# Optimization experiments

Hardware: AMD Instinct MI355X
Metric: run time of the kernel (lower is better)

Reference implementation:

```python
import math
import jax, jax.numpy as jnp
import numpy as np

INPUT_DIM = 512
HIDDEN_DIM = 512
BATCH = 8
SEQ_LEN = 4096


def _xavier(key, shape):
    fan_out, fan_in = shape
    limit = math.sqrt(6.0 / (fan_in + fan_out))
    return jax.random.uniform(key, shape, jnp.float32, -limit, limit)


def setup_inputs() -> dict:
    key = jax.random.key(0)
    kx, kA, kB, kC, kD, kWg = jax.random.split(key, 6)
    return {
        "x": jax.random.normal(kx, (BATCH, SEQ_LEN, INPUT_DIM), jnp.float32),
        "A": jax.random.uniform(kA, (HIDDEN_DIM,), jnp.float32, 0.8, 0.95),
        "B": _xavier(kB, (HIDDEN_DIM, INPUT_DIM)),
        "C": _xavier(kC, (HIDDEN_DIM, HIDDEN_DIM)),
        "D": _xavier(kD, (HIDDEN_DIM, INPUT_DIM)),
        "Wg": _xavier(kWg, (HIDDEN_DIM, INPUT_DIM)),
        "bias_h": jnp.zeros((HIDDEN_DIM,), jnp.float32),
        "bias_y": jnp.zeros((HIDDEN_DIM,), jnp.float32),
    }


def reference(x, A, B, C, D, Wg, bias_h, bias_y):
    # x: (b, t, i). Eval mode: dropout is identity.
    hidden_dim = A.shape[0]
    # Precompute all input-dependent per-step terms as batched GEMMs.
    g = jnp.clip(jax.nn.sigmoid(jnp.einsum('bti,hi->bth', x, Wg)), 0.05, 0.95)
    xB = jnp.einsum('bti,hi->bth', x, B)
    # h_t = h_{t-1} + g_t*(A*h_{t-1} + xB_t + bias_h - h_{t-1})
    #     = (1 - g_t*(1 - A)) * h_{t-1} + g_t*(xB_t + bias_h)
    a_coef = 1.0 - g * (1.0 - A)          # (b, t, h)
    b_coef = g * (xB + bias_h)            # (b, t, h)

    def step(h, ab):
        a_t, b_t = ab
        h = a_t * h + b_t
        return h, h

    h0 = jnp.zeros((x.shape[0], hidden_dim), x.dtype)
    _, hs = jax.lax.scan(step, h0, (jnp.swapaxes(a_coef, 0, 1), jnp.swapaxes(b_coef, 0, 1)))
    hs = jnp.swapaxes(hs, 0, 1)           # (b, t, h)

    scale = 1.0 / math.sqrt(hidden_dim)
    y = (jnp.einsum('bth,oh->bto', hs, C) + jnp.einsum('bti,hi->bth', x, D) + bias_y) * scale
    return y
```

## Files before the change

kernel.cpp:

```cpp
#include <hip/hip_runtime.h>
#include <math.h>

#define MTOT 32768
#define KD 512
#define HD 512
#define NB 8
#define TS 4096
#define NCHUNK 64
#define TCHUNK 64

typedef __attribute__((ext_vector_type(8))) short bf16x8;
typedef __attribute__((ext_vector_type(4))) float f32x4;
typedef __attribute__((ext_vector_type(4))) unsigned short us4;

#define GLD16(gsrc, ldst) __builtin_amdgcn_global_load_lds( \
    (const __attribute__((address_space(1))) void*)(gsrc),   \
    (__attribute__((address_space(3))) void*)(ldst), 16, 0, 0)

__device__ __forceinline__ unsigned short f2bf(float f) {
    unsigned u = __float_as_uint(f);
    return (unsigned short)((u + 0x7FFFu + ((u >> 16) & 1u)) >> 16);
}
__device__ __forceinline__ float bf2f(unsigned short u) {
    return __uint_as_float(((unsigned)u) << 16);
}

__global__ __launch_bounds__(256) void cast_x(const float* __restrict__ src,
                                              unsigned short* __restrict__ dst) {
    const int i = (blockIdx.x * 256 + threadIdx.x) * 4;
    float4 v = *(const float4*)(src + i);
    us4 o; o.x = f2bf(v.x); o.y = f2bf(v.y); o.z = f2bf(v.z); o.w = f2bf(v.w);
    *(us4*)(dst + i) = o;
}

__global__ __launch_bounds__(256) void cast_w(const float* __restrict__ B,
                                              const float* __restrict__ D,
                                              const float* __restrict__ G,
                                              const float* __restrict__ C,
                                              unsigned short* __restrict__ dst) {
    const float* srcs[4] = {B, D, G, C};
    const float* s = srcs[blockIdx.y];
    unsigned short* d = dst + (size_t)blockIdx.y * (HD * KD);
    const int i = (blockIdx.x * 256 + threadIdx.x) * 4;
    float4 v = *(const float4*)(s + i);
    us4 o; o.x = f2bf(v.x); o.y = f2bf(v.y); o.z = f2bf(v.z); o.w = f2bf(v.w);
    *(us4*)(d + i) = o;
}

__global__ __launch_bounds__(256, 2) void in_gemm_mfma(
    const short* __restrict__ xb, const short* __restrict__ wmat,
    const float* __restrict__ Avec, const float* __restrict__ bias_h,
    unsigned* __restrict__ ab16, unsigned short* __restrict__ xd16,
    float2* __restrict__ chPS)
{
    __shared__ __align__(16) short Xs[128 * 64];
    __shared__ __align__(16) short Ws[3][64 * 64];
    const int tid = threadIdx.x;
    const int w = tid >> 6, l = tid & 63;
    const int m0 = blockIdx.x * 128;
    const int n0 = blockIdx.y * 64;
    const int wm = (w & 1) * 64;
    const int wn = (w >> 1) * 32;

    int xsrc[4], xdst[4];
    #pragma unroll
    for (int j = 0; j < 4; ++j) {
        const int s = (w * 4 + j) * 64 + l;
        const int r = s >> 3, g = (s & 7) ^ (r & 7);
        xsrc[j] = (m0 + r) * KD + g * 8;
        xdst[j] = (w * 4 + j) * 64 * 8;
    }
    int wsrc[2], wdst[2];
    #pragma unroll
    for (int j = 0; j < 2; ++j) {
        const int s = (w * 2 + j) * 64 + l;
        const int r = s >> 3, g = (s & 7) ^ (r & 7);
        wsrc[j] = (n0 + r) * KD + g * 8;
        wdst[j] = (w * 2 + j) * 64 * 8;
    }

    f32x4 acc[3][4][2];
    #pragma unroll
    for (int a = 0; a < 3; ++a)
        #pragma unroll
        for (int i = 0; i < 4; ++i)
            #pragma unroll
            for (int j = 0; j < 2; ++j) acc[a][i][j] = (f32x4)0.0f;

    for (int kk = 0; kk < KD; kk += 64) {
        __syncthreads();
        #pragma unroll
        for (int j = 0; j < 4; ++j) GLD16(xb + xsrc[j] + kk, Xs + xdst[j]);
        #pragma unroll
        for (int mat = 0; mat < 3; ++mat)
            #pragma unroll
            for (int j = 0; j < 2; ++j)
                GLD16(wmat + (size_t)mat * (HD * KD) + wsrc[j] + kk, &Ws[mat][wdst[j]]);
        __syncthreads();
        #pragma unroll
        for (int kc = 0; kc < 2; ++kc) {
            const int g = kc * 4 + (l >> 4);
            bf16x8 af[4];
            #pragma unroll
            for (int mt = 0; mt < 4; ++mt) {
                const int r = wm + mt * 16 + (l & 15);
                af[mt] = *(const bf16x8*)(Xs + r * 64 + ((g ^ (r & 7)) * 8));
            }
            #pragma unroll
            for (int mat = 0; mat < 3; ++mat) {
                #pragma unroll
                for (int nt = 0; nt < 2; ++nt) {
                    const int r = wn + nt * 16 + (l & 15);
                    bf16x8 bfv = *(const bf16x8*)(&Ws[mat][r * 64 + ((g ^ (r & 7)) * 8)]);
                    #pragma unroll
                    for (int mt = 0; mt < 4; ++mt)
                        acc[mat][mt][nt] = __builtin_amdgcn_mfma_f32_16x16x32_bf16(
                            af[mt], bfv, acc[mat][mt][nt], 0, 0, 0);
                }
            }
        }
    }

    const int q  = l >> 4;
    const int cl = l & 15;
    const int bidx   = m0 >> 12;
    const int c_in_b = ((m0 & (TS - 1)) >> 6) + (w & 1);
    #pragma unroll
    for (int nt = 0; nt < 2; ++nt) {
        const int n = n0 + wn + nt * 16 + cl;
        const float An1 = 1.0f - Avec[n];
        const float bh  = bias_h[n];
        float Pc = 1.0f, Sc = 0.0f;
        #pragma unroll
        for (int mt = 0; mt < 4; ++mt) {
            float Pl = 1.0f, Sl = 0.0f;
            #pragma unroll
            for (int r = 0; r < 4; ++r) {
                const float vB = acc[0][mt][nt][r];
                const float vG = acc[2][mt][nt][r];
                float g = 1.0f / (1.0f + expf(-vG));
                g = fminf(fmaxf(g, 0.05f), 0.95f);
                const unsigned short su = f2bf(g * An1);
                const unsigned short bu = f2bf(g * (vB + bh));
                const float a  = 1.0f - bf2f(su);
                const float bb = bf2f(bu);
                const int m = m0 + wm + mt * 16 + q * 4 + r;
                const size_t off = (size_t)m * HD + n;
                ab16[off] = (unsigned)su | ((unsigned)bu << 16);
                xd16[off] = f2bf(acc[1][mt][nt][r]);
                Sl = fmaf(a, Sl, bb);
                Pl *= a;
            }
            float Pm = 1.0f, Sm = 0.0f;
            #pragma unroll
            for (int k = 0; k < 4; ++k) {
                const float Pk = __shfl(Pl, cl + 16 * k, 64);
                const float Sk = __shfl(Sl, cl + 16 * k, 64);
                Sm = fmaf(Pk, Sm, Sk);
                Pm *= Pk;
            }
            Sc = fmaf(Pm, Sc, Sm);
            Pc *= Pm;
        }
        if (q == 0) {
            const size_t bh_i = (size_t)bidx * HD + n;
            chPS[bh_i * NCHUNK + c_in_b] = make_float2(Pc, Sc);
        }
    }
}

__global__ __launch_bounds__(256) void scan_pass2(
    const float2* __restrict__ chPS, float* __restrict__ hin)
{
    const int bh = blockIdx.x * blockDim.x + threadIdx.x;
    const float2* p = chPS + (size_t)bh * NCHUNK;
    float h = 0.0f;
    #pragma unroll
    for (int c = 0; c < NCHUNK; ++c) {
        hin[(size_t)c * (NB * HD) + bh] = h;
        const float2 ps = p[c];
        h = fmaf(ps.x, h, ps.y);
    }
}

__global__ __launch_bounds__(256) void scan_pass3(
    const unsigned* __restrict__ ab, const float* __restrict__ hin,
    unsigned short* __restrict__ hs_out)
{
    const int g = blockIdx.x * blockDim.x + threadIdx.x;
    const int h = g & (HD - 1);
    const int rest = g >> 9;
    const int b = rest & (NB - 1);
    const int c = rest >> 3;
    size_t idx = ((size_t)(b * TS + c * TCHUNK)) * HD + h;
    float hv = hin[(size_t)c * (NB * HD) + b * HD + h];
    #pragma unroll 4
    for (int t = 0; t < TCHUNK; ++t) {
        const unsigned v = ab[idx];
        const float a  = 1.0f - bf2f((unsigned short)(v & 0xFFFFu));
        const float bb = bf2f((unsigned short)(v >> 16));
        hv = fmaf(a, hv, bb);
        hs_out[idx] = f2bf(hv);
        idx += HD;
    }
}

__global__ __launch_bounds__(256, 2) void out_gemm_mfma(
    const short* __restrict__ hs, const short* __restrict__ Cb,
    const unsigned short* __restrict__ xd16,
    const float* __restrict__ bias_y, float* __restrict__ y)
{
    __shared__ __align__(16) short Hs[128 * 64];
    __shared__ __align__(16) short Cs[128 * 64];
    const int tid = threadIdx.x;
    const int w = tid >> 6, l = tid & 63;
    const int m0 = blockIdx.x * 128;
    const int n0 = blockIdx.y * 128;
    const int wm = (w & 1) * 64;
    const int wn = (w >> 1) * 64;

    int src_h[4], src_c[4], dst_s[4];
    #pragma unroll
    for (int j = 0; j < 4; ++j) {
        const int s = (w * 4 + j) * 64 + l;
        const int r = s >> 3, g = (s & 7) ^ (r & 7);
        src_h[j] = (m0 + r) * HD + g * 8;
        src_c[j] = (n0 + r) * HD + g * 8;
        dst_s[j] = (w * 4 + j) * 64 * 8;
    }

    f32x4 acc[4][4];
    #pragma unroll
    for (int i = 0; i < 4; ++i)
        #pragma unroll
        for (int j = 0; j < 4; ++j) acc[i][j] = (f32x4)0.0f;

    for (int kk = 0; kk < HD; kk += 64) {
        __syncthreads();
        #pragma unroll
        for (int j = 0; j < 4; ++j) {
            GLD16(hs + src_h[j] + kk, Hs + dst_s[j]);
            GLD16(Cb + src_c[j] + kk, Cs + dst_s[j]);
        }
        __syncthreads();
        #pragma unroll
        for (int kc = 0; kc < 2; ++kc) {
            const int g = kc * 4 + (l >> 4);
            bf16x8 af[4], bfv[4];
            #pragma unroll
            for (int t = 0; t < 4; ++t) {
                const int ra = wm + t * 16 + (l & 15);
                af[t] = *(const bf16x8*)(Hs + ra * 64 + ((g ^ (ra & 7)) * 8));
                const int rb = wn + t * 16 + (l & 15);
                bfv[t] = *(const bf16x8*)(Cs + rb * 64 + ((g ^ (rb & 7)) * 8));
            }
            #pragma unroll
            for (int mt = 0; mt < 4; ++mt)
                #pragma unroll
                for (int nt = 0; nt < 4; ++nt)
                    acc[mt][nt] = __builtin_amdgcn_mfma_f32_16x16x32_bf16(
                        af[mt], bfv[nt], acc[mt][nt], 0, 0, 0);
        }
    }

    const float scale = 0.04419417382415922f;
    #pragma unroll
    for (int nt = 0; nt < 4; ++nt) {
        const int n = n0 + wn + nt * 16 + (l & 15);
        const float by = bias_y[n];
        #pragma unroll
        for (int mt = 0; mt < 4; ++mt) {
            #pragma unroll
            for (int r = 0; r < 4; ++r) {
                const int m = m0 + wm + mt * 16 + (l >> 4) * 4 + r;
                const size_t off = (size_t)m * HD + n;
                y[off] = (acc[mt][nt][r] + bf2f(xd16[off]) + by) * scale;
            }
        }
    }
}

extern "C" void kernel_launch(void* const* d_in, const int* in_sizes, int n_in,
                              void* d_out, int out_size, void* d_ws, size_t ws_size,
                              hipStream_t stream) {
    const float* x      = (const float*)d_in[0];
    const float* Avec   = (const float*)d_in[1];
    const float* Bw     = (const float*)d_in[2];
    const float* Cw     = (const float*)d_in[3];
    const float* Dw     = (const float*)d_in[4];
    const float* Wg     = (const float*)d_in[5];
    const float* bias_h = (const float*)d_in[6];
    const float* bias_y = (const float*)d_in[7];
    float* y = (float*)d_out;

    unsigned* ab16       = (unsigned*)d_ws;
    unsigned short* xd16 = (unsigned short*)(ab16 + (size_t)MTOT * HD);
    unsigned short* x16  = xd16 + (size_t)MTOT * HD;
    unsigned short* w16  = x16 + (size_t)MTOT * HD;
    float2* chPS = (float2*)(w16 + (size_t)4 * HD * KD);
    float* hin   = (float*)(chPS + (size_t)NB * HD * NCHUNK);

    cast_x<<<MTOT * KD / 1024, 256, 0, stream>>>(x, x16);
    cast_w<<<dim3(HD * KD / 1024, 4), 256, 0, stream>>>(Bw, Dw, Wg, Cw, w16);

    in_gemm_mfma<<<dim3(MTOT / 128, HD / 64), 256, 0, stream>>>(
        (const short*)x16, (const short*)w16, Avec, bias_h, ab16, xd16, chPS);

    scan_pass2<<<(NB * HD) / 256, 256, 0, stream>>>(chPS, hin);
    scan_pass3<<<(NB * HD * NCHUNK) / 256, 256, 0, stream>>>(ab16, hin, x16);

    out_gemm_mfma<<<dim3(MTOT / 128, HD / 128), 256, 0, stream>>>(
        (const short*)x16, (const short*)(w16 + (size_t)3 * HD * KD), xd16, bias_y, y);
}
```

Measured before the change: 272.6 us.

## Move xD GEMM into output GEMM, fold chunk-prefix scan into pass3, merge casts

The x·D product is no longer computed in the input GEMM and stored as a bf16 intermediate. It is now accumulated directly in the output GEMM alongside hs·C, which removes a 32K×512 write and read. The separate chunk-carry scan kernel is removed: each pass3 thread recomputes its carry-in serially from the per-chunk (P,S) pairs, which are stored in a new layout. The two cast kernels become one, the sigmoid uses fast exp and rcp, and the input GEMM's occupancy hint rises to 3. The trade-off is that the output GEMM does twice the MFMA work and needs twice the LDS, and the later chunks repeat up to 63 serial loads each.

```diff
diff --git a/kernel.cpp b/kernel.cpp
--- a/kernel.cpp
+++ b/kernel.cpp
@@ -25,36 +25,38 @@
     return __uint_as_float(((unsigned)u) << 16);
 }
 
-__global__ __launch_bounds__(256) void cast_x(const float* __restrict__ src,
-                                              unsigned short* __restrict__ dst) {
-    const int i = (blockIdx.x * 256 + threadIdx.x) * 4;
+__global__ __launch_bounds__(256) void cast_all(
+    const float* __restrict__ x, const float* __restrict__ B,
+    const float* __restrict__ G, const float* __restrict__ C,
+    const float* __restrict__ D,
+    unsigned short* __restrict__ x16, unsigned short* __restrict__ w16)
+{
+    const int blk = blockIdx.x;
+    const float* src;
+    unsigned short* dst;
+    int i;
+    if (blk < (MTOT * KD / 1024)) {
+        src = x; dst = x16;
+        i = blk * 1024 + threadIdx.x * 4;
+    } else {
+        const int r = blk - (MTOT * KD / 1024);
+        const int mat = r >> 8;
+        src = (mat == 0) ? B : (mat == 1) ? G : (mat == 2) ? C : D;
+        dst = w16 + (size_t)mat * (HD * KD);
+        i = (r & 255) * 1024 + threadIdx.x * 4;
+    }
     float4 v = *(const float4*)(src + i);
     us4 o; o.x = f2bf(v.x); o.y = f2bf(v.y); o.z = f2bf(v.z); o.w = f2bf(v.w);
     *(us4*)(dst + i) = o;
 }
 
-__global__ __launch_bounds__(256) void cast_w(const float* __restrict__ B,
-                                              const float* __restrict__ D,
-                                              const float* __restrict__ G,
-                                              const float* __restrict__ C,
-                                              unsigned short* __restrict__ dst) {
-    const float* srcs[4] = {B, D, G, C};
-    const float* s = srcs[blockIdx.y];
-    unsigned short* d = dst + (size_t)blockIdx.y * (HD * KD);
-    const int i = (blockIdx.x * 256 + threadIdx.x) * 4;
-    float4 v = *(const float4*)(s + i);
-    us4 o; o.x = f2bf(v.x); o.y = f2bf(v.y); o.z = f2bf(v.z); o.w = f2bf(v.w);
-    *(us4*)(d + i) = o;
-}
-
-__global__ __launch_bounds__(256, 2) void in_gemm_mfma(
+__global__ __launch_bounds__(256, 3) void in_gemm_mfma(
     const short* __restrict__ xb, const short* __restrict__ wmat,
     const float* __restrict__ Avec, const float* __restrict__ bias_h,
-    unsigned* __restrict__ ab16, unsigned short* __restrict__ xd16,
-    float2* __restrict__ chPS)
+    unsigned* __restrict__ ab16, float2* __restrict__ chPS)
 {
     __shared__ __align__(16) short Xs[128 * 64];
-    __shared__ __align__(16) short Ws[3][64 * 64];
+    __shared__ __align__(16) short Ws[2][64 * 64];
     const int tid = threadIdx.x;
     const int w = tid >> 6, l = tid & 63;
     const int m0 = blockIdx.x * 128;
@@ -79,9 +81,9 @@
         wdst[j] = (w * 2 + j) * 64 * 8;
     }
 
-    f32x4 acc[3][4][2];
-    #pragma unroll
-    for (int a = 0; a < 3; ++a)
+    f32x4 acc[2][4][2];
+    #pragma unroll
+    for (int a = 0; a < 2; ++a)
         #pragma unroll
         for (int i = 0; i < 4; ++i)
             #pragma unroll
@@ -92,7 +94,7 @@
         #pragma unroll
         for (int j = 0; j < 4; ++j) GLD16(xb + xsrc[j] + kk, Xs + xdst[j]);
         #pragma unroll
-        for (int mat = 0; mat < 3; ++mat)
+        for (int mat = 0; mat < 2; ++mat)
             #pragma unroll
             for (int j = 0; j < 2; ++j)
                 GLD16(wmat + (size_t)mat * (HD * KD) + wsrc[j] + kk, &Ws[mat][wdst[j]]);
@@ -107,7 +109,7 @@
                 af[mt] = *(const bf16x8*)(Xs + r * 64 + ((g ^ (r & 7)) * 8));
             }
             #pragma unroll
-            for (int mat = 0; mat < 3; ++mat) {
+            for (int mat = 0; mat < 2; ++mat) {
                 #pragma unroll
                 for (int nt = 0; nt < 2; ++nt) {
                     const int r = wn + nt * 16 + (l & 15);
@@ -137,17 +139,15 @@
             #pragma unroll
             for (int r = 0; r < 4; ++r) {
                 const float vB = acc[0][mt][nt][r];
-                const float vG = acc[2][mt][nt][r];
-                float g = 1.0f / (1.0f + expf(-vG));
+                const float vG = acc[1][mt][nt][r];
+                float g = __builtin_amdgcn_rcpf(1.0f + __expf(-vG));
                 g = fminf(fmaxf(g, 0.05f), 0.95f);
                 const unsigned short su = f2bf(g * An1);
                 const unsigned short bu = f2bf(g * (vB + bh));
                 const float a  = 1.0f - bf2f(su);
                 const float bb = bf2f(bu);
                 const int m = m0 + wm + mt * 16 + q * 4 + r;
-                const size_t off = (size_t)m * HD + n;
-                ab16[off] = (unsigned)su | ((unsigned)bu << 16);
-                xd16[off] = f2bf(acc[1][mt][nt][r]);
+                ab16[(size_t)m * HD + n] = (unsigned)su | ((unsigned)bu << 16);
                 Sl = fmaf(a, Sl, bb);
                 Pl *= a;
             }
@@ -163,28 +163,13 @@
             Pc *= Pm;
         }
         if (q == 0) {
-            const size_t bh_i = (size_t)bidx * HD + n;
-            chPS[bh_i * NCHUNK + c_in_b] = make_float2(Pc, Sc);
-        }
-    }
-}
-
-__global__ __launch_bounds__(256) void scan_pass2(
-    const float2* __restrict__ chPS, float* __restrict__ hin)
-{
-    const int bh = blockIdx.x * blockDim.x + threadIdx.x;
-    const float2* p = chPS + (size_t)bh * NCHUNK;
-    float h = 0.0f;
-    #pragma unroll
-    for (int c = 0; c < NCHUNK; ++c) {
-        hin[(size_t)c * (NB * HD) + bh] = h;
-        const float2 ps = p[c];
-        h = fmaf(ps.x, h, ps.y);
+            chPS[(size_t)c_in_b * (NB * HD) + bidx * HD + n] = make_float2(Pc, Sc);
+        }
     }
 }
 
 __global__ __launch_bounds__(256) void scan_pass3(
-    const unsigned* __restrict__ ab, const float* __restrict__ hin,
+    const unsigned* __restrict__ ab, const float2* __restrict__ chPS,
     unsigned short* __restrict__ hs_out)
 {
     const int g = blockIdx.x * blockDim.x + threadIdx.x;
@@ -192,8 +177,13 @@
     const int rest = g >> 9;
     const int b = rest & (NB - 1);
     const int c = rest >> 3;
+    const float2* p = chPS + (size_t)b * HD + h;
+    float hv = 0.0f;
+    for (int j = 0; j < c; ++j) {
+        const float2 ps = p[(size_t)j * (NB * HD)];
+        hv = fmaf(ps.x, hv, ps.y);
+    }
     size_t idx = ((size_t)(b * TS + c * TCHUNK)) * HD + h;
-    float hv = hin[(size_t)c * (NB * HD) + b * HD + h];
     #pragma unroll 4
     for (int t = 0; t < TCHUNK; ++t) {
         const unsigned v = ab[idx];
@@ -205,13 +195,15 @@
     }
 }
 
-__global__ __launch_bounds__(256, 2) void out_gemm_mfma(
-    const short* __restrict__ hs, const short* __restrict__ Cb,
-    const unsigned short* __restrict__ xd16,
+__global__ __launch_bounds__(256, 2) void out_gemm_dual(
+    const short* __restrict__ hs, const short* __restrict__ xb,
+    const short* __restrict__ Cb, const short* __restrict__ Db,
     const float* __restrict__ bias_y, float* __restrict__ y)
 {
     __shared__ __align__(16) short Hs[128 * 64];
+    __shared__ __align__(16) short Xs2[128 * 64];
     __shared__ __align__(16) short Cs[128 * 64];
+    __shared__ __align__(16) short Ds[128 * 64];
     const int tid = threadIdx.x;
     const int w = tid >> 6, l = tid & 63;
     const int m0 = blockIdx.x * 128;
@@ -219,13 +211,13 @@
     const int wm = (w & 1) * 64;
     const int wn = (w >> 1) * 64;
 
-    int src_h[4], src_c[4], dst_s[4];
+    int src_m[4], src_n[4], dst_s[4];
     #pragma unroll
     for (int j = 0; j < 4; ++j) {
         const int s = (w * 4 + j) * 64 + l;
         const int r = s >> 3, g = (s & 7) ^ (r & 7);
-        src_h[j] = (m0 + r) * HD + g * 8;
-        src_c[j] = (n0 + r) * HD + g * 8;
+        src_m[j] = (m0 + r) * HD + g * 8;
+        src_n[j] = (n0 + r) * HD + g * 8;
         dst_s[j] = (w * 4 + j) * 64 * 8;
     }
 
@@ -239,27 +231,47 @@
         __syncthreads();
         #pragma unroll
         for (int j = 0; j < 4; ++j) {
-            GLD16(hs + src_h[j] + kk, Hs + dst_s[j]);
-            GLD16(Cb + src_c[j] + kk, Cs + dst_s[j]);
+            GLD16(hs + src_m[j] + kk, Hs  + dst_s[j]);
+            GLD16(xb + src_m[j] + kk, Xs2 + dst_s[j]);
+            GLD16(Cb + src_n[j] + kk, Cs  + dst_s[j]);
+            GLD16(Db + src_n[j] + kk, Ds  + dst_s[j]);
         }
         __syncthreads();
         #pragma unroll
         for (int kc = 0; kc < 2; ++kc) {
             const int g = kc * 4 + (l >> 4);
-            bf16x8 af[4], bfv[4];
-            #pragma unroll
-            for (int t = 0; t < 4; ++t) {
-                const int ra = wm + t * 16 + (l & 15);
-                af[t] = *(const bf16x8*)(Hs + ra * 64 + ((g ^ (ra & 7)) * 8));
-                const int rb = wn + t * 16 + (l & 15);
-                bfv[t] = *(const bf16x8*)(Cs + rb * 64 + ((g ^ (rb & 7)) * 8));
-            }
-            #pragma unroll
-            for (int mt = 0; mt < 4; ++mt)
-                #pragma unroll
-                for (int nt = 0; nt < 4; ++nt)
-                    acc[mt][nt] = __builtin_amdgcn_mfma_f32_16x16x32_bf16(
-                        af[mt], bfv[nt], acc[mt][nt], 0, 0, 0);
+            {
+                bf16x8 af[4], bfv[4];
+                #pragma unroll
+                for (int t = 0; t < 4; ++t) {
+                    const int ra = wm + t * 16 + (l & 15);
+                    af[t] = *(const bf16x8*)(Hs + ra * 64 + ((g ^ (ra & 7)) * 8));
+                    const int rb = wn + t * 16 + (l & 15);
+                    bfv[t] = *(const bf16x8*)(Cs + rb * 64 + ((g ^ (rb & 7)) * 8));
+                }
+                #pragma unroll
+                for (int mt = 0; mt < 4; ++mt)
+                    #pragma unroll
+                    for (int nt = 0; nt < 4; ++nt)
+                        acc[mt][nt] = __builtin_amdgcn_mfma_f32_16x16x32_bf16(
+                            af[mt], bfv[nt], acc[mt][nt], 0, 0, 0);
+            }
+            {
+                bf16x8 af[4], bfv[4];
+                #pragma unroll
+                for (int t = 0; t < 4; ++t) {
+                    const int ra = wm + t * 16 + (l & 15);
+                    af[t] = *(const bf16x8*)(Xs2 + ra * 64 + ((g ^ (ra & 7)) * 8));
+                    const int rb = wn + t * 16 + (l & 15);
+                    bfv[t] = *(const bf16x8*)(Ds + rb * 64 + ((g ^ (rb & 7)) * 8));
+                }
+                #pragma unroll
+                for (int mt = 0; mt < 4; ++mt)
+                    #pragma unroll
+                    for (int nt = 0; nt < 4; ++nt)
+                        acc[mt][nt] = __builtin_amdgcn_mfma_f32_16x16x32_bf16(
+                            af[mt], bfv[nt], acc[mt][nt], 0, 0, 0);
+            }
         }
     }
 
@@ -273,8 +285,7 @@
             #pragma unroll
             for (int r = 0; r < 4; ++r) {
                 const int m = m0 + wm + mt * 16 + (l >> 4) * 4 + r;
-                const size_t off = (size_t)m * HD + n;
-                y[off] = (acc[mt][nt][r] + bf2f(xd16[off]) + by) * scale;
+                y[(size_t)m * HD + n] = (acc[mt][nt][r] + by) * scale;
             }
         }
     }
@@ -293,22 +304,22 @@
     const float* bias_y = (const float*)d_in[7];
     float* y = (float*)d_out;
 
-    unsigned* ab16       = (unsigned*)d_ws;
-    unsigned short* xd16 = (unsigned short*)(ab16 + (size_t)MTOT * HD);
-    unsigned short* x16  = xd16 + (size_t)MTOT * HD;
-    unsigned short* w16  = x16 + (size_t)MTOT * HD;
+    unsigned* ab16        = (unsigned*)d_ws;
+    unsigned short* x16   = (unsigned short*)(ab16 + (size_t)MTOT * HD);
+    unsigned short* hs16  = x16 + (size_t)MTOT * HD;
+    unsigned short* w16   = hs16 + (size_t)MTOT * HD;
     float2* chPS = (float2*)(w16 + (size_t)4 * HD * KD);
-    float* hin   = (float*)(chPS + (size_t)NB * HD * NCHUNK);
-
-    cast_x<<<MTOT * KD / 1024, 256, 0, stream>>>(x, x16);
-    cast_w<<<dim3(HD * KD / 1024, 4), 256, 0, stream>>>(Bw, Dw, Wg, Cw, w16);
+
+    cast_all<<<MTOT * KD / 1024 + 4 * (HD * KD / 1024), 256, 0, stream>>>(
+        x, Bw, Wg, Cw, Dw, x16, w16);
 
     in_gemm_mfma<<<dim3(MTOT / 128, HD / 64), 256, 0, stream>>>(
-        (const short*)x16, (const short*)w16, Avec, bias_h, ab16, xd16, chPS);
-
-    scan_pass2<<<(NB * HD) / 256, 256, 0, stream>>>(chPS, hin);
-    scan_pass3<<<(NB * HD * NCHUNK) / 256, 256, 0, stream>>>(ab16, hin, x16);
-
-    out_gemm_mfma<<<dim3(MTOT / 128, HD / 128), 256, 0, stream>>>(
-        (const short*)x16, (const short*)(w16 + (size_t)3 * HD * KD), xd16, bias_y, y);
-}
+        (const short*)x16, (const short*)w16, Avec, bias_h, ab16, chPS);
+
+    scan_pass3<<<(NB * HD * NCHUNK) / 256, 256, 0, stream>>>(ab16, chPS, hs16);
+
+    out_gemm_dual<<<dim3(MTOT / 128, HD / 128), 256, 0, stream>>>(
+        (const short*)hs16, (const short*)x16,
+        (const short*)(w16 + (size_t)2 * HD * KD),
+        (const short*)(w16 + (size_t)3 * HD * KD), bias_y, y);
+}
```

New measurement: 248.9 us. -8.7%, faster.
